# Kernel tuning notes

Measured on AMD Instinct MI355X. Metric: run time of the kernel, lower is better.

Reference implementation:

```python
import jax, jax.numpy as jnp
import numpy as np

IN_H = IN_W = 128
OUT_H = OUT_W = 512
CHUNK = 65536  # = 256*256, same chunk size as the torch while-loop
EPS = 1e-6


def _conv3(x, w, b):
    y = jax.lax.conv_general_dilated(x, w, (1, 1), ((1, 1), (1, 1)),
                                     dimension_numbers=('NCHW', 'OIHW', 'NCHW'))
    return y + b[None, :, None, None]


def _centers(n):
    # torch.arange(-1,1,2/n)+1/n  ==  cell centers in (-1,1)
    return (jnp.arange(n, dtype=jnp.float32) + 0.5) * (2.0 / n) - 1.0


def setup_inputs() -> dict:
    key = jax.random.key(0)
    ks = iter(jax.random.split(key, 40))
    rnd = lambda shape, s: jax.random.normal(next(ks), shape, jnp.float32) * s
    inp = {
        'x': jax.random.uniform(next(ks), (1, 3, IN_H, IN_W), jnp.float32),
        'output_size': jnp.array([OUT_H, OUT_W], dtype=jnp.int32),
        # EDSR encoder params
        'head_w': rnd((64, 3, 3, 3), 0.05), 'head_b': rnd((64,), 0.01),
        'rb_w': rnd((16, 2, 64, 64, 3, 3), 0.02), 'rb_b': rnd((16, 2, 64), 0.01),
        'tail_w': rnd((64, 64, 3, 3), 0.02), 'tail_b': rnd((64,), 0.01),
        # MLP 580 -> 256 -> 256 -> 256 -> 256 -> 3
        'mw0': rnd((580, 256), 0.04), 'mb0': rnd((256,), 0.01),
        'mw1': rnd((256, 256), 0.06), 'mb1': rnd((256,), 0.01),
        'mw2': rnd((256, 256), 0.06), 'mb2': rnd((256,), 0.01),
        'mw3': rnd((256, 256), 0.06), 'mb3': rnd((256,), 0.01),
        'mw4': rnd((256, 3), 0.06), 'mb4': rnd((3,), 0.01),
    }
    return inp


def reference(x, output_size, head_w, head_b, rb_w, rb_b, tail_w, tail_b,
              mw0, mb0, mw1, mb1, mw2, mb2, mw3, mb3, mw4, mb4):
    # ---- EDSR encoder (head conv + 16 resblocks + tail conv, residual) ----
    h0 = _conv3(x, head_w, head_b)

    def block(h, wb):
        w0, b0, w1, b1 = wb
        return h + _conv3(jax.nn.relu(_conv3(h, w0, b0)), w1, b1), None

    hb, _ = jax.lax.scan(block, h0, (rb_w[:, 0], rb_b[:, 0], rb_w[:, 1], rb_b[:, 1]))
    feat64 = h0 + _conv3(hb, tail_w, tail_b)  # [1,64,H,W]
    B, C, H, W = feat64.shape

    # im2col 3x3 pad 1 -> channel order (c, kh, kw), matching torch im2col.view
    p = jnp.pad(feat64, ((0, 0), (0, 0), (1, 1), (1, 1)))
    feat = jnp.stack([p[:, :, i:i + H, j:j + W]
                      for i in range(3) for j in range(3)],
                     axis=2).reshape(B, C * 9, H, W)  # [1,576,H,W]

    # normalized cell-center coordinate map of the feature grid: [2,H,W], (h,w)
    fg = jnp.stack(jnp.meshgrid(_centers(H), _centers(W), indexing='ij'))

    ws = (mw0, mw1, mw2, mw3, mw4)
    bs = (mb0, mb1, mb2, mb3, mb4)

    def mlp(t):
        for w, b in zip(ws[:-1], bs[:-1]):
            t = jax.nn.relu(t @ w + b)
        return t @ ws[-1] + bs[-1]

    dh, dw = 1.0 / H, 1.0 / W
    hw = jnp.array([H, W], jnp.float32)
    q_cell = jnp.array([2.0 * H / OUT_H, 2.0 * W / OUT_W], jnp.float32)
    fimg = feat[0]  # [576,H,W]

    def sample(img, gh, gw):
        # torch grid_sampler nearest, align_corners=False, round-half-to-even
        iy = jnp.clip(jnp.round(((gh + 1.0) * H - 1.0) * 0.5), 0, H - 1).astype(jnp.int32)
        ix = jnp.clip(jnp.round(((gw + 1.0) * W - 1.0) * 0.5), 0, W - 1).astype(jnp.int32)
        return img[:, iy, ix].T  # [P, C]

    def query_chunk(s_grid):  # [P,2] = (h,w) normalized coords
        preds, areas = [], []
        for r in (0, 1):
            for c in (0, 1):
                gh = jnp.clip(s_grid[:, 0] + (2.0 * r - 1.0) * dh, -1 + EPS, 1 - EPS)
                gw = jnp.clip(s_grid[:, 1] + (2.0 * c - 1.0) * dw, -1 + EPS, 1 - EPS)
                q_feat = sample(fimg, gh, gw)            # [P,576]
                q_grid = sample(fg, gh, gw)              # [P,2]
                rel = (s_grid - q_grid) * hw             # [P,2]
                inp = jnp.concatenate(
                    [q_feat, rel, jnp.broadcast_to(q_cell, rel.shape)], axis=-1)
                preds.append(mlp(inp))                   # [P,3]
                areas.append(jnp.abs(rel[:, 0] * rel[:, 1]))
        tot = areas[0] + areas[1] + areas[2] + areas[3] + 1e-9
        # LIIF local ensembling with swapped (diagonal) areas
        num = (preds[0] * areas[3][:, None] + preds[1] * areas[2][:, None]
               + preds[2] * areas[1][:, None] + preds[3] * areas[0][:, None])
        return num / tot[:, None]

    grid = jnp.stack(jnp.meshgrid(_centers(OUT_H), _centers(OUT_W), indexing='ij'),
                     axis=-1).reshape(-1, 2)             # [n,2]
    chunks = grid.reshape(-1, CHUNK, 2)                  # [nc,CHUNK,2]
    ys = jax.lax.map(query_chunk, chunks)                # [nc,CHUNK,3]
    y = ys.reshape(OUT_H, OUT_W, 3).transpose(2, 0, 1)[None]  # [1,3,OH,OW]
    return jnp.clip(y, 0.0, 1.0)
```

## Files before the change

### kernel.cpp

```cpp
#include <hip/hip_runtime.h>
#include <hip/hip_fp16.h>

typedef __attribute__((ext_vector_type(8))) _Float16 half8;
typedef __attribute__((ext_vector_type(4))) _Float16 half4;
typedef __attribute__((ext_vector_type(4))) float float4v;

#define NPIX 16384

__device__ inline half8 h8zero() {
    half8 z = {(_Float16)0, (_Float16)0, (_Float16)0, (_Float16)0,
               (_Float16)0, (_Float16)0, (_Float16)0, (_Float16)0};
    return z;
}

__global__ void pack_all(const float* __restrict__ rb_w, const float* __restrict__ tail_w,
                         const float* __restrict__ mw0, const float* __restrict__ mw1,
                         const float* __restrict__ mw2, const float* __restrict__ mw3,
                         const float* __restrict__ mw4, const float* __restrict__ mb0,
                         const float* __restrict__ x, const float* __restrict__ head_w,
                         const float* __restrict__ head_b,
                         _Float16* __restrict__ pwc, _Float16* __restrict__ pw0,
                         _Float16* __restrict__ pwm, float* __restrict__ b0p,
                         _Float16* __restrict__ h0) {
    int idx = blockIdx.x * 256 + threadIdx.x;
    if (idx < 1216512) {
        int ci = idx / 36864;
        int e  = idx % 36864;
        int j = e & 7, ln = (e >> 3) & 63, kcnt = e >> 9;
        int kc = kcnt % 18, ntc = kcnt / 18;
        int k = kc * 32 + (ln >> 4) * 8 + j;
        int nn = ntc * 16 + (ln & 15);
        int ij = k >> 6, c = k & 63;
        const float* src = (ci < 32) ? (rb_w + ci * 36864) : tail_w;
        pwc[idx] = (_Float16)src[(nn * 64 + c) * 9 + ij];
        return;
    }
    idx -= 1216512;
    if (idx < 147456) {
        int j = idx & 7, ln = (idx >> 3) & 63, kcnt = idx >> 9;
        int kc = kcnt % 18, ntc = kcnt / 18;
        int k = kc * 32 + (ln >> 4) * 8 + j;
        int nn = ntc * 16 + (ln & 15);
        int ij = k >> 6, c = k & 63;
        pw0[idx] = (_Float16)mw0[(c * 9 + ij) * 256 + nn];
        return;
    }
    idx -= 147456;
    if (idx < 200704) {
        if (idx < 196608) {
            int l = idx / 65536;
            int e = idx % 65536;
            int j = e & 7, ln = (e >> 3) & 63, kcnt = e >> 9;
            int kc = kcnt & 7, ntc = kcnt >> 3;
            int k = kc * 32 + (ln >> 4) * 8 + j;
            int nn = ntc * 16 + (ln & 15);
            const float* w = (l == 0) ? mw1 : ((l == 1) ? mw2 : mw3);
            pwm[idx] = (_Float16)w[k * 256 + nn];
        } else {
            int e = idx - 196608;
            int j = e & 7, ln = (e >> 3) & 63, kc = e >> 9;
            int k = kc * 32 + (ln >> 4) * 8 + j;
            int nn = ln & 15;
            pwm[idx] = (nn < 3) ? (_Float16)mw4[k * 3 + nn] : (_Float16)0.0f;
        }
        return;
    }
    idx -= 200704;
    if (idx < 256) {
        b0p[idx] = mb0[idx] + 0.5f * (mw0[578 * 256 + idx] + mw0[579 * 256 + idx]);
        return;
    }
    idx -= 256;
    if (idx < NPIX * 64) {
        int o = idx & 63, p = idx >> 6;
        int py = p >> 7, px = p & 127;
        float acc = head_b[o];
        #pragma unroll
        for (int c = 0; c < 3; ++c)
            #pragma unroll
            for (int i = 0; i < 3; ++i)
                #pragma unroll
                for (int jj = 0; jj < 3; ++jj) {
                    int y = py + i - 1, xx = px + jj - 1;
                    if (y >= 0 && y < 128 && xx >= 0 && xx < 128)
                        acc += x[c * 16384 + y * 128 + xx]
                             * head_w[((o * 3 + c) * 3 + i) * 3 + jj];
                }
        h0[idx] = (_Float16)acc;
    }
}

#define LDS_STRIDE 72

template <int DH, int DW, int SW, int SOFF, int RES>
__device__ __forceinline__ void conv_stage(
    const _Float16* __restrict__ src, _Float16* __restrict__ dst, _Float16* __restrict__ INb,
    const _Float16* __restrict__ pw, const float* __restrict__ bias,
    int q, int r, int nb, int gy0, int gx0, _Float16* __restrict__ gout)
{
    half8 B[18];
    #pragma unroll
    for (int kc = 0; kc < 18; ++kc)
        B[kc] = *(const half8*)(pw + ((((nb >> 4) * 18 + kc) * 64 + (q << 4) + r) << 3));
    float bv = bias[nb + r];
    constexpr int NPXc = DH * DW;
    constexpr int NT = (NPXc + 15) >> 4;
    #pragma unroll 1
    for (int tl = 0; tl < NT; ++tl) {
        int pa = tl * 16 + r;
        int ca = pa < NPXc ? pa : NPXc - 1;
        int my = ca / DW, mx = ca % DW;
        float4v acc = {0.f, 0.f, 0.f, 0.f};
        #pragma unroll
        for (int kc = 0; kc < 18; ++kc) {
            int ij = kc >> 1;
            int di = ij / 3 - 1;
            int dj = ij % 3 - 1;
            int cb = ((kc & 1) << 5) + (q << 3);
            int sp = (my + 1 + di + SOFF) * SW + (mx + 1 + dj + SOFF);
            half8 a = *(const half8*)(src + sp * LDS_STRIDE + cb);
            acc = __builtin_amdgcn_mfma_f32_16x16x32_f16(a, B[kc], acc, 0, 0, 0);
        }
        #pragma unroll
        for (int reg = 0; reg < 4; ++reg) {
            int pc = tl * 16 + (q << 2) + reg;
            if (pc >= NPXc) continue;
            int dy = pc / DW, dx = pc % DW;
            int gy = gy0 + dy, gx = gx0 + dx;
            bool valid = (gy >= 0 && gy < 128 && gx >= 0 && gx < 128);
            if (RES == 0) {
                float v = fmaxf(acc[reg] + bv, 0.f);
                dst[pc * LDS_STRIDE + nb + r] = valid ? (_Float16)v : (_Float16)0.0f;
            } else if (RES == 1) {
                int sl = ((dy + 2) * 16 + dx + 2) * LDS_STRIDE + nb + r;
                float v = acc[reg] + bv + (float)INb[sl];
                INb[sl] = valid ? (_Float16)v : (_Float16)0.0f;
            } else {
                int sl = ((dy + 4) * 16 + dx + 4) * LDS_STRIDE + nb + r;
                float v = acc[reg] + bv + (float)INb[sl];
                gout[(((gy << 7) + gx) << 6) + nb + r] = (_Float16)v;
            }
        }
    }
}

__global__ __launch_bounds__(256, 3)
void rb_pair(const _Float16* __restrict__ img, const _Float16* __restrict__ pw,
             const float* __restrict__ bias, _Float16* __restrict__ out) {
    __shared__ _Float16 IN[192 * LDS_STRIDE];
    __shared__ _Float16 MID[140 * LDS_STRIDE];
    int t = threadIdx.x;
    int wave = t >> 6, lane = t & 63, q = lane >> 4, r = lane & 15;
    int tr = blockIdx.x >> 4, tc = blockIdx.x & 15;
    int ty0 = tr << 2, tx0 = tc << 3;
    int nb = wave << 4;

    #pragma unroll
    for (int i = 0; i < 6; ++i) {
        int idx = t + i * 256;
        int px = idx >> 3, c = idx & 7;
        int iy = px >> 4, ix = px & 15;
        int gy = ty0 - 4 + iy, gx = tx0 - 4 + ix;
        half8 v = h8zero();
        if (gy >= 0 && gy < 128 && gx >= 0 && gx < 128)
            v = *(const half8*)(img + (((gy << 7) + gx) << 6) + (c << 3));
        *(half8*)(IN + px * LDS_STRIDE + (c << 3)) = v;
    }
    __syncthreads();

    conv_stage<10, 14, 16, 0, 0>(IN, MID, IN, pw, bias, q, r, nb, ty0 - 3, tx0 - 3, nullptr);
    __syncthreads();
    conv_stage<8, 12, 14, 0, 1>(MID, nullptr, IN, pw + 36864, bias + 64, q, r, nb,
                                ty0 - 2, tx0 - 2, nullptr);
    __syncthreads();
    conv_stage<6, 10, 16, 2, 0>(IN, MID, IN, pw + 2 * 36864, bias + 128, q, r, nb,
                                ty0 - 1, tx0 - 1, nullptr);
    __syncthreads();
    conv_stage<4, 8, 10, 0, 2>(MID, nullptr, IN, pw + 3 * 36864, bias + 192, q, r, nb,
                               ty0, tx0, out);
}

template <int NTOT, int MTPER, bool RELU, bool RES, bool F32OUT>
__global__ __launch_bounds__(256, 2)
void conv_mfma_r(const _Float16* __restrict__ img, const _Float16* __restrict__ pw,
                 const float* __restrict__ bias, const _Float16* res,
                 _Float16* outh, float* outf) {
    int wave = threadIdx.x >> 6, lane = threadIdx.x & 63;
    int q = lane >> 4, r = lane & 15;
    int nt, mt0;
    if constexpr (NTOT == 4) {
        nt = wave;
        mt0 = blockIdx.x * MTPER;
    } else {
        nt = (blockIdx.x & 3) * 4 + wave;
        mt0 = (blockIdx.x >> 2) * MTPER;
    }
    half8 B[18];
    #pragma unroll
    for (int kc = 0; kc < 18; ++kc)
        B[kc] = *(const half8*)(pw + (((nt * 18 + kc) * 64 + lane) << 3));
    int n = nt * 16 + r;
    float bv = bias[n];
    #pragma unroll
    for (int mi = 0; mi < MTPER; ++mi) {
        int mt = mt0 + mi;
        int p0 = mt * 16;
        int py = p0 >> 7;
        int pxl = (p0 & 127) + r;
        float4v acc = {0.f, 0.f, 0.f, 0.f};
        #pragma unroll
        for (int kc = 0; kc < 18; ++kc) {
            int ij = kc >> 1;
            int di = ij / 3 - 1;
            int dj = ij % 3 - 1;
            int cb = ((kc & 1) << 5) + (q << 3);
            int yy = py + di, xx = pxl + dj;
            half8 a = h8zero();
            if (yy >= 0 && yy < 128 && xx >= 0 && xx < 128)
                a = *(const half8*)(img + (((yy << 7) + xx) << 6) + cb);
            acc = __builtin_amdgcn_mfma_f32_16x16x32_f16(a, B[kc], acc, 0, 0, 0);
        }
        #pragma unroll
        for (int reg = 0; reg < 4; ++reg) {
            int p = p0 + (q << 2) + reg;
            float v = acc[reg] + bv;
            if (RES) v += (float)res[p * (NTOT * 16) + n];
            if (RELU) v = fmaxf(v, 0.f);
            if (F32OUT) outf[p * (NTOT * 16) + n] = v;
            else        outh[p * (NTOT * 16) + n] = (_Float16)v;
        }
    }
}

__global__ __launch_bounds__(512, 4)
void mlp_kernel(const float* __restrict__ apre, const float* __restrict__ mw0,
                const float* __restrict__ mb1, const float* __restrict__ mb2,
                const float* __restrict__ mb3, const float* __restrict__ mb4,
                const _Float16* __restrict__ pwm, const _Float16* __restrict__ pw4,
                float* __restrict__ out) {
    __shared__ _Float16 act[32768];
    __shared__ float sArea[128], sRelH[128], sRelW[128];
    __shared__ int sCell[128];
    __shared__ float sWh[256], sWw[256];

    int t = threadIdx.x;
    int bid = blockIdx.x;
    int logical = (bid & 7) * 1024 + (bid >> 3);
    int p0 = logical << 5;

    if (t < 128) {
        int lp = t >> 2, rc = t & 3;
        int p = p0 + lp;
        int oh = p >> 9, ow = p & 511;
        float sh = (oh + 0.5f) * (2.0f / 512.0f) - 1.0f;
        float sw = (ow + 0.5f) * (2.0f / 512.0f) - 1.0f;
        float gh = sh + (((rc >> 1) != 0) ? (1.0f / 128.0f) : (-1.0f / 128.0f));
        float gw = sw + (((rc & 1) != 0) ? (1.0f / 128.0f) : (-1.0f / 128.0f));
        const float lim = 1.0f - 1e-6f;
        gh = fminf(fmaxf(gh, -lim), lim);
        gw = fminf(fmaxf(gw, -lim), lim);
        int iy = (int)rintf(((gh + 1.0f) * 128.0f - 1.0f) * 0.5f);
        int ix = (int)rintf(((gw + 1.0f) * 128.0f - 1.0f) * 0.5f);
        iy = iy < 0 ? 0 : (iy > 127 ? 127 : iy);
        ix = ix < 0 ? 0 : (ix > 127 ? 127 : ix);
        float cy = (iy + 0.5f) * (2.0f / 128.0f) - 1.0f;
        float cx = (ix + 0.5f) * (2.0f / 128.0f) - 1.0f;
        float rh = (sh - cy) * 128.0f;
        float rw = (sw - cx) * 128.0f;
        sCell[t] = (iy << 7) + ix;
        sRelH[t] = rh; sRelW[t] = rw;
        sArea[t] = fabsf(rh * rw);
    }
    if (t < 256) {
        sWh[t] = mw0[576 * 256 + t];
        sWw[t] = mw0[577 * 256 + t];
    }
    __syncthreads();

    int wave = t >> 6, lane = t & 63, q = lane >> 4, r = lane & 15;

    {
        int s = (wave << 4) + r;
        float rh = sRelH[s], rw = sRelW[s];
        const float* ap = apre + ((size_t)sCell[s] << 8) + (q << 3);
        #pragma unroll
        for (int j = 0; j < 8; ++j) {
            int f0 = (j << 5) + (q << 3);
            float4v lo = *(const float4v*)(ap + (j << 5));
            float4v hi = *(const float4v*)(ap + (j << 5) + 4);
            half8 hv;
            #pragma unroll
            for (int kk = 0; kk < 4; ++kk) {
                float v = lo[kk] + rh * sWh[f0 + kk] + rw * sWw[f0 + kk];
                hv[kk] = (_Float16)fmaxf(v, 0.0f);
            }
            #pragma unroll
            for (int kk = 0; kk < 4; ++kk) {
                float v = hi[kk] + rh * sWh[f0 + 4 + kk] + rw * sWw[f0 + 4 + kk];
                hv[4 + kk] = (_Float16)fmaxf(v, 0.0f);
            }
            *(half8*)(act + ((((wave << 3) + j) * 64 + lane) << 3)) = hv;
        }
    }
    __syncthreads();

    float4v acc[2][8];
    #pragma unroll 1
    for (int l = 0; l < 3; ++l) {
        #pragma unroll
        for (int mti = 0; mti < 2; ++mti)
            #pragma unroll
            for (int nts = 0; nts < 8; ++nts)
                acc[mti][nts] = (float4v){0.f, 0.f, 0.f, 0.f};
        const _Float16* pw = pwm + l * 65536;
        for (int kc = 0; kc < 8; ++kc) {
            half8 A0 = *(const half8*)(pw + ((((wave * 2 + 0) * 8 + kc) * 64 + lane) << 3));
            half8 A1 = *(const half8*)(pw + ((((wave * 2 + 1) * 8 + kc) * 64 + lane) << 3));
            half8 Bf[4];
            #pragma unroll
            for (int nts = 0; nts < 4; ++nts)
                Bf[nts] = *(const half8*)(act + ((((nts << 3) + kc) * 64 + lane) << 3));
            #pragma unroll
            for (int nts = 0; nts < 4; ++nts) {
                acc[0][nts] = __builtin_amdgcn_mfma_f32_16x16x32_f16(A0, Bf[nts], acc[0][nts], 0, 0, 0);
                acc[1][nts] = __builtin_amdgcn_mfma_f32_16x16x32_f16(A1, Bf[nts], acc[1][nts], 0, 0, 0);
            }
            #pragma unroll
            for (int nts = 0; nts < 4; ++nts)
                Bf[nts] = *(const half8*)(act + (((((nts + 4) << 3) + kc) * 64 + lane) << 3));
            #pragma unroll
            for (int nts = 0; nts < 4; ++nts) {
                acc[0][nts + 4] = __builtin_amdgcn_mfma_f32_16x16x32_f16(A0, Bf[nts], acc[0][nts + 4], 0, 0, 0);
                acc[1][nts + 4] = __builtin_amdgcn_mfma_f32_16x16x32_f16(A1, Bf[nts], acc[1][nts + 4], 0, 0, 0);
            }
        }
        const float* mb = (l == 0) ? mb1 : ((l == 1) ? mb2 : mb3);
        __syncthreads();
        #pragma unroll
        for (int mti = 0; mti < 2; ++mti) {
            float4v bvv = *(const float4v*)(mb + (wave << 5) + mti * 16 + (q << 2));
            #pragma unroll
            for (int nts = 0; nts < 8; ++nts) {
                int base = ((((nts << 3) + wave) * 64
                             + ((mti * 2 + (q >> 1)) << 4) + r) << 3) + ((q & 1) << 2);
                half4 hv;
                #pragma unroll
                for (int reg = 0; reg < 4; ++reg)
                    hv[reg] = (_Float16)fmaxf(acc[mti][nts][reg] + bvv[reg], 0.0f);
                *(half4*)(act + base) = hv;
            }
        }
        __syncthreads();
    }

    {
        float4v af = {0.f, 0.f, 0.f, 0.f};
        #pragma unroll
        for (int kc = 0; kc < 8; ++kc) {
            half8 A = *(const half8*)(pw4 + ((kc * 64 + lane) << 3));
            half8 Bf = *(const half8*)(act + ((((wave << 3) + kc) * 64 + lane) << 3));
            af = __builtin_amdgcn_mfma_f32_16x16x32_f16(A, Bf, af, 0, 0, 0);
        }
        int s = (wave << 4) + r;
        int lp = s >> 2, rc = s & 3;
        float ar = sArea[(lp << 2) + (3 - rc)];
        float c0 = (af[0] + mb4[0]) * ar;
        float c1 = (af[1] + mb4[1]) * ar;
        float c2 = (af[2] + mb4[2]) * ar;
        c0 += __shfl_xor(c0, 1); c1 += __shfl_xor(c1, 1); c2 += __shfl_xor(c2, 1);
        float at = ar + __shfl_xor(ar, 1);
        c0 += __shfl_xor(c0, 2); c1 += __shfl_xor(c1, 2); c2 += __shfl_xor(c2, 2);
        at += __shfl_xor(at, 2);
        if (q == 0 && rc == 0) {
            float inv = 1.0f / (at + 1e-9f);
            out[p0 + lp]          = fminf(fmaxf(c0 * inv, 0.0f), 1.0f);
            out[262144 + p0 + lp] = fminf(fmaxf(c1 * inv, 0.0f), 1.0f);
            out[524288 + p0 + lp] = fminf(fmaxf(c2 * inv, 0.0f), 1.0f);
        }
    }
}

extern "C" void kernel_launch(void* const* d_in, const int* in_sizes, int n_in,
                              void* d_out, int out_size, void* d_ws, size_t ws_size,
                              hipStream_t stream) {
    (void)in_sizes; (void)n_in; (void)out_size; (void)ws_size;
    const float* x      = (const float*)d_in[0];
    const float* head_w = (const float*)d_in[2];
    const float* head_b = (const float*)d_in[3];
    const float* rb_w   = (const float*)d_in[4];
    const float* rb_b   = (const float*)d_in[5];
    const float* tail_w = (const float*)d_in[6];
    const float* tail_b = (const float*)d_in[7];
    const float* mw0    = (const float*)d_in[8];
    const float* mb0    = (const float*)d_in[9];
    const float* mw1    = (const float*)d_in[10];
    const float* mb1    = (const float*)d_in[11];
    const float* mw2    = (const float*)d_in[12];
    const float* mb2    = (const float*)d_in[13];
    const float* mw3    = (const float*)d_in[14];
    const float* mb3    = (const float*)d_in[15];
    const float* mw4    = (const float*)d_in[16];
    const float* mb4    = (const float*)d_in[17];
    float* out = (float*)d_out;

    char* w = (char*)d_ws;
    auto take = [&](size_t n) { char* p = w; w += (n + 255) & ~(size_t)255; return p; };
    _Float16* pwc  = (_Float16*)take(33u * 36864u * 2u);
    _Float16* pw0  = (_Float16*)take(147456u * 2u);
    _Float16* pwm  = (_Float16*)take(200704u * 2u);
    float*    b0p  = (float*)take(256u * 4u);
    _Float16* h0   = (_Float16*)take((size_t)NPIX * 64u * 2u);
    _Float16* hbuf = (_Float16*)take((size_t)NPIX * 64u * 2u);
    _Float16* tbuf = (_Float16*)take((size_t)NPIX * 64u * 2u);
    _Float16* feat = (_Float16*)take((size_t)NPIX * 64u * 2u);
    float*    apre = (float*)take((size_t)NPIX * 256u * 4u);

    pack_all<<<10209, 256, 0, stream>>>(rb_w, tail_w, mw0, mw1, mw2, mw3, mw4, mb0,
                                        x, head_w, head_b, pwc, pw0, pwm, b0p, h0);

    const _Float16* cur = h0;
    for (int p = 0; p < 8; ++p) {
        _Float16* dst = (p & 1) ? tbuf : hbuf;
        rb_pair<<<512, 256, 0, stream>>>(cur, pwc + 4 * p * 36864, rb_b + p * 256, dst);
        cur = dst;
    }
    conv_mfma_r<4, 2, false, true, false><<<512, 256, 0, stream>>>(
        cur, pwc + 32 * 36864, tail_b, h0, feat, nullptr);
    conv_mfma_r<16, 4, false, false, true><<<1024, 256, 0, stream>>>(
        feat, pw0, b0p, nullptr, nullptr, apre);

    mlp_kernel<<<8192, 512, 0, stream>>>(apre, mw0, mb1, mb2, mb3, mb4,
                                         pwm, pwm + 196608, out);
}
```

Before: 755.3 us.

## Fuse four residual blocks per kernel with 8x8 tiles and wider halo

Replaces the two-resblock fused kernel with a four-resblock fused kernel, so the residual trunk launches 4 kernels instead of 8 and each 64-channel activation makes half as many global round trips. Each block now handles an 8x8 output tile with an 8-pixel halo held in LDS, using 512 threads split into 4 N-tiles times 2 M-halves. The cost is much more redundant halo recompute (22x22 down to 8x8 across eight conv stages), only 256 blocks at one block per CU, and a large LDS footprint.

```diff
diff --git a/kernel.cpp b/kernel.cpp
--- a/kernel.cpp
+++ b/kernel.cpp
@@ -92,24 +92,26 @@
 
 #define LDS_STRIDE 72
 
-template <int DH, int DW, int SW, int SOFF, int RES>
-__device__ __forceinline__ void conv_stage(
-    const _Float16* __restrict__ src, _Float16* __restrict__ dst, _Float16* __restrict__ INb,
+template <int S, int SW, int SOFF, int RES, int ROFF>
+__device__ __forceinline__ void qconv_stage(
+    const _Float16* __restrict__ src, _Float16* __restrict__ dst,
+    _Float16* __restrict__ INb,
     const _Float16* __restrict__ pw, const float* __restrict__ bias,
-    int q, int r, int nb, int gy0, int gx0, _Float16* __restrict__ gout)
+    int q, int r, int nt, int mhalf, int gy0, int gx0, _Float16* __restrict__ gout)
 {
     half8 B[18];
     #pragma unroll
     for (int kc = 0; kc < 18; ++kc)
-        B[kc] = *(const half8*)(pw + ((((nb >> 4) * 18 + kc) * 64 + (q << 4) + r) << 3));
+        B[kc] = *(const half8*)(pw + (((nt * 18 + kc) * 64 + (q << 4) + r) << 3));
+    int nb = nt << 4;
     float bv = bias[nb + r];
-    constexpr int NPXc = DH * DW;
+    constexpr int NPXc = S * S;
     constexpr int NT = (NPXc + 15) >> 4;
     #pragma unroll 1
-    for (int tl = 0; tl < NT; ++tl) {
+    for (int tl = mhalf; tl < NT; tl += 2) {
         int pa = tl * 16 + r;
         int ca = pa < NPXc ? pa : NPXc - 1;
-        int my = ca / DW, mx = ca % DW;
+        int my = ca / S, mx = ca % S;
         float4v acc = {0.f, 0.f, 0.f, 0.f};
         #pragma unroll
         for (int kc = 0; kc < 18; ++kc) {
@@ -125,18 +127,18 @@
         for (int reg = 0; reg < 4; ++reg) {
             int pc = tl * 16 + (q << 2) + reg;
             if (pc >= NPXc) continue;
-            int dy = pc / DW, dx = pc % DW;
+            int dy = pc / S, dx = pc % S;
             int gy = gy0 + dy, gx = gx0 + dx;
             bool valid = (gy >= 0 && gy < 128 && gx >= 0 && gx < 128);
             if (RES == 0) {
                 float v = fmaxf(acc[reg] + bv, 0.f);
                 dst[pc * LDS_STRIDE + nb + r] = valid ? (_Float16)v : (_Float16)0.0f;
             } else if (RES == 1) {
-                int sl = ((dy + 2) * 16 + dx + 2) * LDS_STRIDE + nb + r;
+                int sl = ((dy + ROFF) * 24 + dx + ROFF) * LDS_STRIDE + nb + r;
                 float v = acc[reg] + bv + (float)INb[sl];
                 INb[sl] = valid ? (_Float16)v : (_Float16)0.0f;
             } else {
-                int sl = ((dy + 4) * 16 + dx + 4) * LDS_STRIDE + nb + r;
+                int sl = ((dy + ROFF) * 24 + dx + ROFF) * LDS_STRIDE + nb + r;
                 float v = acc[reg] + bv + (float)INb[sl];
                 gout[(((gy << 7) + gx) << 6) + nb + r] = (_Float16)v;
             }
@@ -144,23 +146,23 @@
     }
 }
 
-__global__ __launch_bounds__(256, 3)
-void rb_pair(const _Float16* __restrict__ img, const _Float16* __restrict__ pw,
+__global__ __launch_bounds__(512, 1)
+void rb_quad(const _Float16* __restrict__ img, const _Float16* __restrict__ pw,
              const float* __restrict__ bias, _Float16* __restrict__ out) {
-    __shared__ _Float16 IN[192 * LDS_STRIDE];
-    __shared__ _Float16 MID[140 * LDS_STRIDE];
+    __shared__ _Float16 IN[576 * LDS_STRIDE];
+    __shared__ _Float16 MID[484 * LDS_STRIDE];
     int t = threadIdx.x;
     int wave = t >> 6, lane = t & 63, q = lane >> 4, r = lane & 15;
+    int nt = wave & 3, mhalf = wave >> 2;
     int tr = blockIdx.x >> 4, tc = blockIdx.x & 15;
-    int ty0 = tr << 2, tx0 = tc << 3;
-    int nb = wave << 4;
+    int ty0 = tr << 3, tx0 = tc << 3;
 
     #pragma unroll
-    for (int i = 0; i < 6; ++i) {
-        int idx = t + i * 256;
+    for (int i = 0; i < 9; ++i) {
+        int idx = t + i * 512;
         int px = idx >> 3, c = idx & 7;
-        int iy = px >> 4, ix = px & 15;
-        int gy = ty0 - 4 + iy, gx = tx0 - 4 + ix;
+        int iy = px / 24, ix = px % 24;
+        int gy = ty0 - 8 + iy, gx = tx0 - 8 + ix;
         half8 v = h8zero();
         if (gy >= 0 && gy < 128 && gx >= 0 && gx < 128)
             v = *(const half8*)(img + (((gy << 7) + gx) << 6) + (c << 3));
@@ -168,16 +170,29 @@
     }
     __syncthreads();
 
-    conv_stage<10, 14, 16, 0, 0>(IN, MID, IN, pw, bias, q, r, nb, ty0 - 3, tx0 - 3, nullptr);
-    __syncthreads();
-    conv_stage<8, 12, 14, 0, 1>(MID, nullptr, IN, pw + 36864, bias + 64, q, r, nb,
-                                ty0 - 2, tx0 - 2, nullptr);
-    __syncthreads();
-    conv_stage<6, 10, 16, 2, 0>(IN, MID, IN, pw + 2 * 36864, bias + 128, q, r, nb,
-                                ty0 - 1, tx0 - 1, nullptr);
-    __syncthreads();
-    conv_stage<4, 8, 10, 0, 2>(MID, nullptr, IN, pw + 3 * 36864, bias + 192, q, r, nb,
-                               ty0, tx0, out);
+    qconv_stage<22, 24, 0, 0, 0>(IN, MID, IN, pw, bias, q, r, nt, mhalf,
+                                 ty0 - 7, tx0 - 7, nullptr);
+    __syncthreads();
+    qconv_stage<20, 22, 0, 1, 2>(MID, MID, IN, pw + 36864, bias + 64, q, r, nt, mhalf,
+                                 ty0 - 6, tx0 - 6, nullptr);
+    __syncthreads();
+    qconv_stage<18, 24, 2, 0, 0>(IN, MID, IN, pw + 2 * 36864, bias + 128, q, r, nt, mhalf,
+                                 ty0 - 5, tx0 - 5, nullptr);
+    __syncthreads();
+    qconv_stage<16, 18, 0, 1, 4>(MID, MID, IN, pw + 3 * 36864, bias + 192, q, r, nt, mhalf,
+                                 ty0 - 4, tx0 - 4, nullptr);
+    __syncthreads();
+    qconv_stage<14, 24, 4, 0, 0>(IN, MID, IN, pw + 4 * 36864, bias + 256, q, r, nt, mhalf,
+                                 ty0 - 3, tx0 - 3, nullptr);
+    __syncthreads();
+    qconv_stage<12, 14, 0, 1, 6>(MID, MID, IN, pw + 5 * 36864, bias + 320, q, r, nt, mhalf,
+                                 ty0 - 2, tx0 - 2, nullptr);
+    __syncthreads();
+    qconv_stage<10, 24, 6, 0, 0>(IN, MID, IN, pw + 6 * 36864, bias + 384, q, r, nt, mhalf,
+                                 ty0 - 1, tx0 - 1, nullptr);
+    __syncthreads();
+    qconv_stage<8, 10, 0, 2, 8>(MID, MID, IN, pw + 7 * 36864, bias + 448, q, r, nt, mhalf,
+                                ty0, tx0, out);
 }
 
 template <int NTOT, int MTPER, bool RELU, bool RES, bool F32OUT>
@@ -419,9 +434,9 @@
                                         x, head_w, head_b, pwc, pw0, pwm, b0p, h0);
 
     const _Float16* cur = h0;
-    for (int p = 0; p < 8; ++p) {
+    for (int p = 0; p < 4; ++p) {
         _Float16* dst = (p & 1) ? tbuf : hbuf;
-        rb_pair<<<512, 256, 0, stream>>>(cur, pwc + 4 * p * 36864, rb_b + p * 256, dst);
+        rb_quad<<<256, 512, 0, stream>>>(cur, pwc + 8 * p * 36864, rb_b + p * 512, dst);
         cur = dst;
     }
     conv_mfma_r<4, 2, false, true, false><<<512, 256, 0, stream>>>(
```

After: 791.4 us. 1.05x slower.

## Fuse last residual block pair with tail conv in one halo-tiled kernel

Applied to the files above, without the earlier changes.

Adds an rb_tail kernel that runs the final two residual blocks and the tail convolution (with the global h0 skip) on an 18x12 halo tile held in LDS. It replaces the eighth rb_pair launch and the separate tail conv kernel, cutting one launch and a full feature-map round trip through global memory. In exchange it recomputes a larger halo (five stacked convs), uses more LDS, and lowers the occupancy hint to 2 blocks per CU.

```diff
diff --git a/kernel.cpp b/kernel.cpp
--- a/kernel.cpp
+++ b/kernel.cpp
@@ -92,9 +92,10 @@
 
 #define LDS_STRIDE 72
 
-template <int DH, int DW, int SW, int SOFF, int RES>
+template <int DH, int DW, int SW, int SOFF, int RES, int ROFF, int INW>
 __device__ __forceinline__ void conv_stage(
-    const _Float16* __restrict__ src, _Float16* __restrict__ dst, _Float16* __restrict__ INb,
+    const _Float16* __restrict__ src, _Float16* __restrict__ dst,
+    _Float16* __restrict__ INb, const _Float16* __restrict__ resg,
     const _Float16* __restrict__ pw, const float* __restrict__ bias,
     int q, int r, int nb, int gy0, int gx0, _Float16* __restrict__ gout)
 {
@@ -132,12 +133,15 @@
                 float v = fmaxf(acc[reg] + bv, 0.f);
                 dst[pc * LDS_STRIDE + nb + r] = valid ? (_Float16)v : (_Float16)0.0f;
             } else if (RES == 1) {
-                int sl = ((dy + 2) * 16 + dx + 2) * LDS_STRIDE + nb + r;
+                int sl = ((dy + ROFF) * INW + dx + ROFF) * LDS_STRIDE + nb + r;
                 float v = acc[reg] + bv + (float)INb[sl];
                 INb[sl] = valid ? (_Float16)v : (_Float16)0.0f;
+            } else if (RES == 2) {
+                int sl = ((dy + ROFF) * INW + dx + ROFF) * LDS_STRIDE + nb + r;
+                float v = acc[reg] + bv + (float)INb[sl];
+                gout[(((gy << 7) + gx) << 6) + nb + r] = (_Float16)v;
             } else {
-                int sl = ((dy + 4) * 16 + dx + 4) * LDS_STRIDE + nb + r;
-                float v = acc[reg] + bv + (float)INb[sl];
+                float v = acc[reg] + bv + (float)resg[(((gy << 7) + gx) << 6) + nb + r];
                 gout[(((gy << 7) + gx) << 6) + nb + r] = (_Float16)v;
             }
         }
@@ -168,16 +172,60 @@
     }
     __syncthreads();
 
-    conv_stage<10, 14, 16, 0, 0>(IN, MID, IN, pw, bias, q, r, nb, ty0 - 3, tx0 - 3, nullptr);
-    __syncthreads();
-    conv_stage<8, 12, 14, 0, 1>(MID, nullptr, IN, pw + 36864, bias + 64, q, r, nb,
-                                ty0 - 2, tx0 - 2, nullptr);
-    __syncthreads();
-    conv_stage<6, 10, 16, 2, 0>(IN, MID, IN, pw + 2 * 36864, bias + 128, q, r, nb,
-                                ty0 - 1, tx0 - 1, nullptr);
-    __syncthreads();
-    conv_stage<4, 8, 10, 0, 2>(MID, nullptr, IN, pw + 3 * 36864, bias + 192, q, r, nb,
-                               ty0, tx0, out);
+    conv_stage<10, 14, 16, 0, 0, 0, 16>(IN, MID, IN, nullptr, pw, bias, q, r, nb,
+                                        ty0 - 3, tx0 - 3, nullptr);
+    __syncthreads();
+    conv_stage<8, 12, 14, 0, 1, 2, 16>(MID, nullptr, IN, nullptr, pw + 36864, bias + 64,
+                                       q, r, nb, ty0 - 2, tx0 - 2, nullptr);
+    __syncthreads();
+    conv_stage<6, 10, 16, 2, 0, 0, 16>(IN, MID, IN, nullptr, pw + 2 * 36864, bias + 128,
+                                       q, r, nb, ty0 - 1, tx0 - 1, nullptr);
+    __syncthreads();
+    conv_stage<4, 8, 10, 0, 2, 4, 16>(MID, nullptr, IN, nullptr, pw + 3 * 36864, bias + 192,
+                                      q, r, nb, ty0, tx0, out);
+}
+
+__global__ __launch_bounds__(256, 2)
+void rb_tail(const _Float16* __restrict__ img, const _Float16* __restrict__ h0res,
+             const _Float16* __restrict__ pw, const float* __restrict__ bias,
+             const float* __restrict__ tail_b, _Float16* __restrict__ out) {
+    __shared__ _Float16 IN[252 * LDS_STRIDE];
+    __shared__ _Float16 MID[192 * LDS_STRIDE];
+    int t = threadIdx.x;
+    int wave = t >> 6, lane = t & 63, q = lane >> 4, r = lane & 15;
+    int tr = blockIdx.x >> 4, tc = blockIdx.x & 15;
+    int ty0 = tr << 2, tx0 = tc << 3;
+    int nb = wave << 4;
+
+    #pragma unroll
+    for (int i = 0; i < 8; ++i) {
+        int idx = t + i * 256;
+        if (idx < 2016) {
+            int px = idx >> 3, c = idx & 7;
+            int iy = px / 18, ix = px % 18;
+            int gy = ty0 - 5 + iy, gx = tx0 - 5 + ix;
+            half8 v = h8zero();
+            if (gy >= 0 && gy < 128 && gx >= 0 && gx < 128)
+                v = *(const half8*)(img + (((gy << 7) + gx) << 6) + (c << 3));
+            *(half8*)(IN + px * LDS_STRIDE + (c << 3)) = v;
+        }
+    }
+    __syncthreads();
+
+    conv_stage<12, 16, 18, 0, 0, 0, 18>(IN, MID, IN, nullptr, pw, bias, q, r, nb,
+                                        ty0 - 4, tx0 - 4, nullptr);
+    __syncthreads();
+    conv_stage<10, 14, 16, 0, 1, 2, 18>(MID, nullptr, IN, nullptr, pw + 36864, bias + 64,
+                                        q, r, nb, ty0 - 3, tx0 - 3, nullptr);
+    __syncthreads();
+    conv_stage<8, 12, 18, 2, 0, 0, 18>(IN, MID, IN, nullptr, pw + 2 * 36864, bias + 128,
+                                       q, r, nb, ty0 - 2, tx0 - 2, nullptr);
+    __syncthreads();
+    conv_stage<6, 10, 12, 0, 1, 4, 18>(MID, nullptr, IN, nullptr, pw + 3 * 36864, bias + 192,
+                                       q, r, nb, ty0 - 1, tx0 - 1, nullptr);
+    __syncthreads();
+    conv_stage<4, 8, 18, 4, 3, 0, 18>(IN, nullptr, IN, h0res, pw + 4 * 36864, tail_b,
+                                      q, r, nb, ty0, tx0, out);
 }
 
 template <int NTOT, int MTPER, bool RELU, bool RES, bool F32OUT>
@@ -419,13 +467,13 @@
                                         x, head_w, head_b, pwc, pw0, pwm, b0p, h0);
 
     const _Float16* cur = h0;
-    for (int p = 0; p < 8; ++p) {
+    for (int p = 0; p < 7; ++p) {
         _Float16* dst = (p & 1) ? tbuf : hbuf;
         rb_pair<<<512, 256, 0, stream>>>(cur, pwc + 4 * p * 36864, rb_b + p * 256, dst);
         cur = dst;
     }
-    conv_mfma_r<4, 2, false, true, false><<<512, 256, 0, stream>>>(
-        cur, pwc + 32 * 36864, tail_b, h0, feat, nullptr);
+    rb_tail<<<512, 256, 0, stream>>>(cur, h0, pwc + 28 * 36864, rb_b + 7 * 256,
+                                     tail_b, feat);
     conv_mfma_r<16, 4, false, false, true><<<1024, 256, 0, stream>>>(
         feat, pw0, b0p, nullptr, nullptr, apre);
 
```

Result: no change. 758.7 us (median of 2 runs) (+0.4%).
